# Kernel optimization log

Hardware: AMD Instinct MI355X
Metric: run time of the kernel (lower is better)

Reference implementation:

```python
import jax, jax.numpy as jnp
import numpy as np
from jax import lax


def conv_valid_relu(x, w, b):
    # NHWC valid conv, stride 1, + bias + relu (matches keras Conv2D(..., activation='relu'))
    y = lax.conv_general_dilated(x, w, (1, 1), 'VALID',
                                 dimension_numbers=('NHWC', 'HWIO', 'NHWC'))
    return jax.nn.relu(y + b)


def maxpool2(x):
    # keras MaxPooling2D(): pool 2x2, stride 2, VALID
    return lax.reduce_window(x, -jnp.inf, lax.max, (1, 2, 2, 1), (1, 2, 2, 1), 'VALID')


def affine_bilinear(img, theta):
    # img: [H, W, C]; theta: [6] = (a0..a5).
    # tf.raw_ops.ImageProjectiveTransformV3 semantics (a6=a7=0):
    #   x_in = a0*x_out + a1*y_out + a2;  y_in = a3*x_out + a4*y_out + a5
    # BILINEAR interp; each of the 4 neighbor reads returns fill_value(=0) if out of bounds.
    H, W, C = img.shape
    a0, a1, a2, a3, a4, a5 = theta
    ys, xs = jnp.meshgrid(jnp.arange(H, dtype=img.dtype),
                          jnp.arange(W, dtype=img.dtype), indexing='ij')
    xq = a0 * xs + a1 * ys + a2  # [H, W]
    yq = a3 * xs + a4 * ys + a5
    x0 = jnp.floor(xq)
    y0 = jnp.floor(yq)
    dx = xq - x0
    dy = yq - y0

    def read(yi, xi):
        valid = (yi >= 0) & (yi <= H - 1) & (xi >= 0) & (xi <= W - 1)
        yc = jnp.clip(yi, 0, H - 1).astype(jnp.int32)
        xc = jnp.clip(xi, 0, W - 1).astype(jnp.int32)
        v = img[yc, xc]  # gather -> [H, W, C]
        return jnp.where(valid[..., None], v, jnp.zeros((), img.dtype))

    v00 = read(y0, x0)
    v01 = read(y0, x0 + 1)
    v10 = read(y0 + 1, x0)
    v11 = read(y0 + 1, x0 + 1)
    top = v00 * (1 - dx)[..., None] + v01 * dx[..., None]
    bot = v10 * (1 - dx)[..., None] + v11 * dx[..., None]
    return top * (1 - dy)[..., None] + bot * dy[..., None]


def reference(x, conv1_w, conv1_b, conv2_w, conv2_b, fc_w, fc_b):
    y = conv_valid_relu(x, conv1_w, conv1_b)   # [B,218,218,8]
    y = maxpool2(y)                            # [B,109,109,8]
    y = conv_valid_relu(y, conv2_w, conv2_b)   # [B,105,105,10]
    y = maxpool2(y)                            # [B,52,52,10]
    feat = y.reshape(y.shape[0], -1)           # row-major HWC flatten == keras Flatten
    theta = feat @ fc_w + fc_b                 # [B,6]
    return jax.vmap(affine_bilinear)(x, theta)


def setup_inputs() -> dict:
    key = jax.random.key(0)
    ks = jax.random.split(key, 6)
    B, H, W, C = 64, 224, 224, 3
    flat_dim = 52 * 52 * 10  # from 224 -> conv7 -> pool -> conv5 -> pool
    x = jax.random.normal(ks[0], (B, H, W, C), dtype=jnp.float32)
    conv1_w = jax.random.normal(ks[1], (7, 7, 3, 8), dtype=jnp.float32) * 0.05
    conv1_b = jnp.zeros((8,), jnp.float32)
    conv2_w = jax.random.normal(ks[2], (5, 5, 8, 10), dtype=jnp.float32) * 0.05
    conv2_b = jnp.zeros((10,), jnp.float32)
    # keras init: kernel zeros, bias = identity affine. Add tiny noise to kernel so the
    # predicted transform actually varies per image (exercises the resampler).
    fc_w = jax.random.normal(ks[3], (flat_dim, 6), dtype=jnp.float32) * 1e-4
    fc_b = jnp.array([1.0, 0.0, 0.0, 0.0, 1.0, 0.0], dtype=jnp.float32)
    return {"x": x, "conv1_w": conv1_w, "conv1_b": conv1_b,
            "conv2_w": conv2_w, "conv2_b": conv2_b, "fc_w": fc_w, "fc_b": fc_b}
```

## Files before the change

### kernel.cpp

```cpp
#include <hip/hip_runtime.h>
#include <math.h>

#define BATCH 64
#define HI 224
#define WI 224
#define P1H 109
#define P1W 109
#define P2H 52
#define P2W 52

typedef _Float16 f16;
typedef _Float16 f16x4 __attribute__((ext_vector_type(4)));
typedef _Float16 f16x8 __attribute__((ext_vector_type(8)));
typedef float    f32x4 __attribute__((ext_vector_type(4)));

#define MFMA16F(a,b,c) __builtin_amdgcn_mfma_f32_16x16x32_f16((a),(b),(c),0,0,0)

#define PROWS 4
#define NROWG 28
#define SROWS 14
#define ROWSH 896
#define STOT  (SROWS*ROWSH)
#define SPAD  12576
#define NBVAR 8
__global__ __launch_bounds__(256) void conv1_kernel(
    const float* __restrict__ x, const float* __restrict__ w1,
    const float* __restrict__ b1,
    f16* __restrict__ p1)
{
    __shared__ f16 smem[SPAD + NBVAR*16*32];
    f16* sh_a = smem;
    f16* sh_b = smem + SPAD;

    const int tid  = threadIdx.x;
    const int lane = tid & 63;
    const int wave = tid >> 6;
    const int bph  = blockIdx.x;
    const int b    = blockIdx.y;
    const int ph0  = PROWS*bph;
    const int ir0  = 2*ph0;

    for (int i = tid; i < NBVAR*16*32; i += 256) sh_b[i] = (f16)0.f;
    __syncthreads();

    for (int i = tid; i < 1176; i += 256) {
        const float v = w1[i];
        const int co = i & 7;
        const int t3 = i >> 3;
        const int ci = t3 % 3;
        const int kk = t3 / 3;
        const int kh = kk / 7;
        const int kw = kk - kh*7;
        const f16 val = (f16)v;
        sh_b[(kh*16     + co  )*32 + kw*4 + ci] = val;
        sh_b[((kh+1)*16 + co+8)*32 + kw*4 + ci] = val;
    }

    for (int u = wave; u < 25; u += 4) {
        const int q = u*512 + lane*8;
        if (q >= SPAD) continue;
        const int row  = q / ROWSH;
        const int rem  = q - row*ROWSH;
        const int col0 = rem >> 2;
        const int ira  = ir0 + row;
        float f0=0.f,f1=0.f,f2=0.f,f3=0.f,f4=0.f,f5=0.f;
        if (q < STOT && ira < HI) {
            const float* src = x + ((size_t)(b*HI + ira)*WI + col0)*3;
            const float2 a = *(const float2*)(src);
            const float2 c = *(const float2*)(src+2);
            const float2 e = *(const float2*)(src+4);
            f0=a.x; f1=a.y; f2=c.x; f3=c.y; f4=e.x; f5=e.y;
        }
        f16x8 hv;
        hv[0]=(f16)f0; hv[1]=(f16)f1; hv[2]=(f16)f2; hv[3]=(f16)0.f;
        hv[4]=(f16)f3; hv[5]=(f16)f4; hv[6]=(f16)f5; hv[7]=(f16)0.f;
        *(f16x8*)(sh_a + q) = hv;
    }
    __syncthreads();

    const int n16 = lane & 15;
    const int g   = lane >> 4;

    f16x8 bv[NBVAR];
#pragma unroll
    for (int v = 0; v < NBVAR; ++v)
        bv[v] = *(const f16x8*)(sh_b + (v*16 + n16)*32 + g*8);
    const float bias = b1[n16 & 7];

    for (int t = wave; t < 14; t += 4) {
        const int abase = (t*16 + n16)*4 + g*8;
        f32x4 acc[4];
#pragma unroll
        for (int q = 0; q < 4; ++q) acc[q] = (f32x4){0.f,0.f,0.f,0.f};

#pragma unroll
        for (int ir = 0; ir < SROWS; ++ir) {
            const int sb = ir*ROWSH + abase;
            const f16x4 h0 = *(const f16x4*)(sh_a + sb);
            const f16x4 h1 = *(const f16x4*)(sh_a + sb + 4);
            const f16x8 ah = __builtin_shufflevector(h0,h1,0,1,2,3,4,5,6,7);
#pragma unroll
            for (int q = 0; q < 4; ++q) {
                const int v = ir - 2*q;
                if (v >= 0 && v < NBVAR)
                    acc[q] = MFMA16F(ah, bv[v], acc[q]);
            }
        }

#pragma unroll
        for (int pr = 0; pr < PROWS; ++pr) {
            const float h0 = fmaxf(acc[pr][0], acc[pr][1]);
            const float h1 = fmaxf(acc[pr][2], acc[pr][3]);
            const float v0 = fmaxf(h0, __shfl_xor(h0, 8));
            const float v1 = fmaxf(h1, __shfl_xor(h1, 8));
            const int ph = ph0 + pr;
            if (n16 < 8 && ph < P1H) {
                const int pc0 = t*8 + 2*g;
                const size_t rbase = ((size_t)(b*P1H + ph))*P1W*8;
                if (pc0 < P1W)
                    p1[rbase + (size_t)pc0*8 + n16] = (f16)fmaxf(v0 + bias, 0.f);
                if (pc0+1 < P1W)
                    p1[rbase + (size_t)(pc0+1)*8 + n16] = (f16)fmaxf(v1 + bias, 0.f);
            }
        }
    }
}

#define C2A 6144
__global__ __launch_bounds__(256) void conv2_kernel(
    const f16* __restrict__ p1,
    const float* __restrict__ w2, const float* __restrict__ b2,
    float* __restrict__ p2)
{
    __shared__ f16 smem[C2A + 16*224];
    f16* sh_a = smem;
    f16* sh_b = smem + C2A;

    const int tid = threadIdx.x;
    const int ph  = blockIdx.x;
    const int b   = blockIdx.y;

    for (int i = tid; i < 16*224; i += 256) sh_b[i] = (f16)0.f;
    for (int i = tid; i < C2A - 5232; i += 256) sh_a[5232 + i] = (f16)0.f;
    __syncthreads();

    for (int i = tid; i < 2000; i += 256) {
        const float v = w2[i];
        const int kh = i / 400;
        int rem = i - kh*400;
        const int kw = rem / 80;
        rem -= kw*80;
        const int ci = rem / 10;
        const int co = rem - ci*10;
        sh_b[co*224 + kh*40 + kw*8 + ci] = (f16)v;
    }

    const size_t gbase = ((size_t)b*P1H + 2*ph) * (P1W*8);
    const ulong2* gsrc = (const ulong2*)(p1 + gbase);
    ulong2* gdst = (ulong2*)sh_a;
    for (int c = tid; c < 654; c += 256) gdst[c] = gsrc[c];
    __syncthreads();

    const int lane = tid & 63;
    const int wave = tid >> 6;
    const int n16  = lane & 15;
    const int g    = lane >> 4;

    f16x8 bh[7];
#pragma unroll
    for (int j = 0; j < 7; ++j)
        bh[j] = *(const f16x8*)(sh_b + n16*224 + j*32 + g*8);
    const float bias = (n16 < 10) ? b2[n16] : 0.f;

    int koff[7];
#pragma unroll
    for (int j = 0; j < 7; ++j) {
        const int chunk = 4*j + g;
        const int kh = chunk / 5;
        const int kw = chunk - kh*5;
        koff[j] = kh*872 + kw*8;
    }

    for (int t = wave; t < 7; t += 4) {
        const int c0 = t*16;
        const int pbase = (c0 + n16)*8;
        float res[2][4];
#pragma unroll
        for (int ro = 0; ro < 2; ++ro) {
            f32x4 accA = {0.f,0.f,0.f,0.f};
            f32x4 accB = {0.f,0.f,0.f,0.f};
            const int rb = ro*872 + pbase;
#pragma unroll
            for (int j = 0; j < 7; ++j) {
                const int si = rb + koff[j];
                const f16x8 ah = *(const f16x8*)(sh_a + si);
                if (j & 1) accB = MFMA16F(ah, bh[j], accB);
                else       accA = MFMA16F(ah, bh[j], accA);
            }
#pragma unroll
            for (int r = 0; r < 4; ++r) res[ro][r] = accA[r] + accB[r];
        }
        if (n16 < 10) {
#pragma unroll
            for (int q = 0; q < 2; ++q) {
                const int pc = (c0 >> 1) + 2*g + q;
                if (pc < P2W) {
                    float m = fmaxf(fmaxf(res[0][2*q], res[0][2*q+1]),
                                    fmaxf(res[1][2*q], res[1][2*q+1]));
                    p2[((size_t)((b*P2H + ph)*P2W) + pc)*10 + n16] = fmaxf(m + bias, 0.f);
                }
            }
        }
    }
}

#define FCSL 16
#define FCCH 1690
__global__ __launch_bounds__(256) void fcA_kernel(
    const float* __restrict__ p2, const float* __restrict__ fw,
    float* __restrict__ partial)
{
    const int s = blockIdx.x;
    const int b = blockIdx.y;
    const int base = s * FCCH;
    const float* f = p2 + (size_t)b*27040;
    float acc[6] = {0.f,0.f,0.f,0.f,0.f,0.f};
    for (int i = threadIdx.x; i < FCCH; i += 256) {
        const float v = f[base + i];
        const float* wp = fw + (size_t)(base + i)*6;
#pragma unroll
        for (int k = 0; k < 6; ++k) acc[k] = fmaf(v, wp[k], acc[k]);
    }
    __shared__ float red[4][6];
#pragma unroll
    for (int k = 0; k < 6; ++k) {
        float v = acc[k];
        for (int off = 32; off > 0; off >>= 1) v += __shfl_down(v, off);
        if ((threadIdx.x & 63) == 0) red[threadIdx.x >> 6][k] = v;
    }
    __syncthreads();
    if (threadIdx.x < 6) {
        const int k = threadIdx.x;
        partial[(b*FCSL + s)*6 + k] = red[0][k] + red[1][k] + red[2][k] + red[3][k];
    }
}

__global__ __launch_bounds__(384) void fcB_kernel(
    const float* __restrict__ partial, const float* __restrict__ fb,
    float* __restrict__ theta)
{
    const int t = threadIdx.x;
    const int b = t / 6, k = t - b*6;
    float s = fb[k];
#pragma unroll
    for (int j = 0; j < FCSL; ++j) s += partial[(b*FCSL + j)*6 + k];
    theta[b*6 + k] = s;
}

__global__ __launch_bounds__(256) void resample_kernel(
    const float* __restrict__ x, const float* __restrict__ theta,
    float* __restrict__ out)
{
    const int idx = blockIdx.x * 256 + threadIdx.x;
    const int total = BATCH * HI * WI;
    if (idx >= total) return;
    const int b   = idx / (HI*WI);
    const int pix = idx - b * (HI*WI);
    const int yo  = pix / WI;
    const int xo  = pix - yo * WI;

    const float* t = theta + b*6;
    const float a0 = t[0], a1 = t[1], a2 = t[2], a3 = t[3], a4 = t[4], a5 = t[5];

    const float fx = (float)xo, fy = (float)yo;
    const float xq = a0*fx + a1*fy + a2;
    const float yq = a3*fx + a4*fy + a5;
    const float x0f = floorf(xq), y0f = floorf(yq);
    const float dx = xq - x0f, dy = yq - y0f;
    const int x0 = (int)x0f, y0 = (int)y0f;

    const float* img = x + (size_t)b * (HI*WI*3);

    const int x1 = x0 + 1, y1 = y0 + 1;
    const bool vx0 = (x0 >= 0) && (x0 <= WI-1);
    const bool vx1 = (x1 >= 0) && (x1 <= WI-1);
    const bool vy0 = (y0 >= 0) && (y0 <= HI-1);
    const bool vy1 = (y1 >= 0) && (y1 <= HI-1);
    const int xc0 = min(max(x0, 0), WI-1);
    const int xc1 = min(max(x1, 0), WI-1);
    const int yc0 = min(max(y0, 0), HI-1);
    const int yc1 = min(max(y1, 0), HI-1);
    const float* p00 = img + (size_t)(yc0*WI + xc0)*3;
    const float* p01 = img + (size_t)(yc0*WI + xc1)*3;
    const float* p10 = img + (size_t)(yc1*WI + xc0)*3;
    const float* p11 = img + (size_t)(yc1*WI + xc1)*3;
    const float m00 = (vy0 && vx0) ? 1.f : 0.f;
    const float m01 = (vy0 && vx1) ? 1.f : 0.f;
    const float m10 = (vy1 && vx0) ? 1.f : 0.f;
    const float m11 = (vy1 && vx1) ? 1.f : 0.f;

    float* op = out + (size_t)idx * 3;
#pragma unroll
    for (int c = 0; c < 3; ++c) {
        const float v00 = m00 * p00[c];
        const float v01 = m01 * p01[c];
        const float v10 = m10 * p10[c];
        const float v11 = m11 * p11[c];
        const float top = v00 * (1.f - dx) + v01 * dx;
        const float bot = v10 * (1.f - dx) + v11 * dx;
        op[c] = top * (1.f - dy) + bot * dy;
    }
}

extern "C" void kernel_launch(void* const* d_in, const int* in_sizes, int n_in,
                              void* d_out, int out_size, void* d_ws, size_t ws_size,
                              hipStream_t stream) {
    const float* x   = (const float*)d_in[0];
    const float* w1  = (const float*)d_in[1];
    const float* b1  = (const float*)d_in[2];
    const float* w2  = (const float*)d_in[3];
    const float* b2  = (const float*)d_in[4];
    const float* fw  = (const float*)d_in[5];
    const float* fb  = (const float*)d_in[6];
    float* out = (float*)d_out;

    char* ws = (char*)d_ws;
    f16*  p1      = (f16*)ws;
    float* p2     = (float*)(ws + 12166144);
    float* partial= (float*)(ws + 19088384);
    float* th     = (float*)(ws + 19113000 - 19113000 % 256 + 256);

    conv1_kernel<<<dim3(NROWG, BATCH), 256, 0, stream>>>(x, w1, b1, p1);
    conv2_kernel<<<dim3(P2H, BATCH), 256, 0, stream>>>(p1, w2, b2, p2);
    fcA_kernel<<<dim3(FCSL, BATCH), 256, 0, stream>>>(p2, fw, partial);
    fcB_kernel<<<dim3(1), 384, 0, stream>>>(partial, fb, th);

    const int total_pix = BATCH * HI * WI;
    resample_kernel<<<dim3((total_pix + 255)/256), 256, 0, stream>>>(x, th, out);
}
```

Measured before the change: 73.41 us.

## Stage conv outputs in shared memory and vectorize resample stores

conv1 and conv2 now write their pooled outputs into shared memory, then copy each row to global memory with 16-byte coalesced stores, replacing scattered 2-byte and 4-byte stores. The resample kernel now has each thread compute four consecutive pixels and write twelve floats as three float4 stores, with one image-aligned grid per batch. This trades an extra barrier and some shared-memory staging for better global-store efficiency. conv1 reuses the weight region of shared memory for output staging, so it needs an added sync after the weights are read into registers.

```diff
diff --git a/kernel.cpp b/kernel.cpp
--- a/kernel.cpp
+++ b/kernel.cpp
@@ -8,6 +8,7 @@
 #define P1W 109
 #define P2H 52
 #define P2W 52
+#define NPIX (HI*WI)
 
 typedef _Float16 f16;
 typedef _Float16 f16x4 __attribute__((ext_vector_type(4)));
@@ -29,8 +30,9 @@
     f16* __restrict__ p1)
 {
     __shared__ f16 smem[SPAD + NBVAR*16*32];
-    f16* sh_a = smem;
-    f16* sh_b = smem + SPAD;
+    f16* sh_a   = smem;
+    f16* sh_b   = smem + SPAD;
+    f16* sh_out = smem + SPAD;
 
     const int tid  = threadIdx.x;
     const int lane = tid & 63;
@@ -86,6 +88,7 @@
     for (int v = 0; v < NBVAR; ++v)
         bv[v] = *(const f16x8*)(sh_b + (v*16 + n16)*32 + g*8);
     const float bias = b1[n16 & 7];
+    __syncthreads();
 
     for (int t = wave; t < 14; t += 4) {
         const int abase = (t*16 + n16)*4 + g*8;
@@ -113,16 +116,24 @@
             const float h1 = fmaxf(acc[pr][2], acc[pr][3]);
             const float v0 = fmaxf(h0, __shfl_xor(h0, 8));
             const float v1 = fmaxf(h1, __shfl_xor(h1, 8));
-            const int ph = ph0 + pr;
-            if (n16 < 8 && ph < P1H) {
+            if (n16 < 8) {
                 const int pc0 = t*8 + 2*g;
-                const size_t rbase = ((size_t)(b*P1H + ph))*P1W*8;
                 if (pc0 < P1W)
-                    p1[rbase + (size_t)pc0*8 + n16] = (f16)fmaxf(v0 + bias, 0.f);
+                    sh_out[(pr*P1W + pc0)*8 + n16] = (f16)fmaxf(v0 + bias, 0.f);
                 if (pc0+1 < P1W)
-                    p1[rbase + (size_t)(pc0+1)*8 + n16] = (f16)fmaxf(v1 + bias, 0.f);
+                    sh_out[(pr*P1W + pc0+1)*8 + n16] = (f16)fmaxf(v1 + bias, 0.f);
             }
         }
+    }
+    __syncthreads();
+
+    for (int c = tid; c < PROWS*P1W; c += 256) {
+        const int pr = c / P1W;
+        const int pc = c - pr*P1W;
+        const int ph = ph0 + pr;
+        if (ph < P1H)
+            *(ulong2*)(p1 + ((size_t)(b*P1H + ph)*P1W + pc)*8) =
+                *(const ulong2*)(sh_out + c*8);
     }
 }
 
@@ -133,8 +144,10 @@
     float* __restrict__ p2)
 {
     __shared__ f16 smem[C2A + 16*224];
+    __shared__ float4 sh_o4[130];
     f16* sh_a = smem;
     f16* sh_b = smem + C2A;
+    float* sh_o = (float*)sh_o4;
 
     const int tid = threadIdx.x;
     const int ph  = blockIdx.x;
@@ -207,11 +220,15 @@
                 if (pc < P2W) {
                     float m = fmaxf(fmaxf(res[0][2*q], res[0][2*q+1]),
                                     fmaxf(res[1][2*q], res[1][2*q+1]));
-                    p2[((size_t)((b*P2H + ph)*P2W) + pc)*10 + n16] = fmaxf(m + bias, 0.f);
+                    sh_o[pc*10 + n16] = fmaxf(m + bias, 0.f);
                 }
             }
         }
     }
+    __syncthreads();
+
+    float4* dst = (float4*)(p2 + (size_t)(b*P2H + ph)*520);
+    for (int i = tid; i < 130; i += 256) dst[i] = sh_o4[i];
 }
 
 #define FCSL 16
@@ -261,55 +278,63 @@
     const float* __restrict__ x, const float* __restrict__ theta,
     float* __restrict__ out)
 {
-    const int idx = blockIdx.x * 256 + threadIdx.x;
-    const int total = BATCH * HI * WI;
-    if (idx >= total) return;
-    const int b   = idx / (HI*WI);
-    const int pix = idx - b * (HI*WI);
-    const int yo  = pix / WI;
-    const int xo  = pix - yo * WI;
+    const int u   = blockIdx.x;
+    const int b   = u / 49;
+    const int blk = u - b*49;
+    const int pix0 = blk*1024 + threadIdx.x*4;
 
     const float* t = theta + b*6;
     const float a0 = t[0], a1 = t[1], a2 = t[2], a3 = t[3], a4 = t[4], a5 = t[5];
-
-    const float fx = (float)xo, fy = (float)yo;
-    const float xq = a0*fx + a1*fy + a2;
-    const float yq = a3*fx + a4*fy + a5;
-    const float x0f = floorf(xq), y0f = floorf(yq);
-    const float dx = xq - x0f, dy = yq - y0f;
-    const int x0 = (int)x0f, y0 = (int)y0f;
-
-    const float* img = x + (size_t)b * (HI*WI*3);
-
-    const int x1 = x0 + 1, y1 = y0 + 1;
-    const bool vx0 = (x0 >= 0) && (x0 <= WI-1);
-    const bool vx1 = (x1 >= 0) && (x1 <= WI-1);
-    const bool vy0 = (y0 >= 0) && (y0 <= HI-1);
-    const bool vy1 = (y1 >= 0) && (y1 <= HI-1);
-    const int xc0 = min(max(x0, 0), WI-1);
-    const int xc1 = min(max(x1, 0), WI-1);
-    const int yc0 = min(max(y0, 0), HI-1);
-    const int yc1 = min(max(y1, 0), HI-1);
-    const float* p00 = img + (size_t)(yc0*WI + xc0)*3;
-    const float* p01 = img + (size_t)(yc0*WI + xc1)*3;
-    const float* p10 = img + (size_t)(yc1*WI + xc0)*3;
-    const float* p11 = img + (size_t)(yc1*WI + xc1)*3;
-    const float m00 = (vy0 && vx0) ? 1.f : 0.f;
-    const float m01 = (vy0 && vx1) ? 1.f : 0.f;
-    const float m10 = (vy1 && vx0) ? 1.f : 0.f;
-    const float m11 = (vy1 && vx1) ? 1.f : 0.f;
-
-    float* op = out + (size_t)idx * 3;
-#pragma unroll
-    for (int c = 0; c < 3; ++c) {
-        const float v00 = m00 * p00[c];
-        const float v01 = m01 * p01[c];
-        const float v10 = m10 * p10[c];
-        const float v11 = m11 * p11[c];
-        const float top = v00 * (1.f - dx) + v01 * dx;
-        const float bot = v10 * (1.f - dx) + v11 * dx;
-        op[c] = top * (1.f - dy) + bot * dy;
-    }
+    const float* img = x + (size_t)b * (NPIX*3);
+
+    float o[12];
+#pragma unroll
+    for (int p = 0; p < 4; ++p) {
+        const int pix = pix0 + p;
+        const int yo  = pix / WI;
+        const int xo  = pix - yo * WI;
+
+        const float fx = (float)xo, fy = (float)yo;
+        const float xq = a0*fx + a1*fy + a2;
+        const float yq = a3*fx + a4*fy + a5;
+        const float x0f = floorf(xq), y0f = floorf(yq);
+        const float dx = xq - x0f, dy = yq - y0f;
+        const int x0 = (int)x0f, y0 = (int)y0f;
+
+        const int x1 = x0 + 1, y1 = y0 + 1;
+        const bool vx0 = (x0 >= 0) && (x0 <= WI-1);
+        const bool vx1 = (x1 >= 0) && (x1 <= WI-1);
+        const bool vy0 = (y0 >= 0) && (y0 <= HI-1);
+        const bool vy1 = (y1 >= 0) && (y1 <= HI-1);
+        const int xc0 = min(max(x0, 0), WI-1);
+        const int xc1 = min(max(x1, 0), WI-1);
+        const int yc0 = min(max(y0, 0), HI-1);
+        const int yc1 = min(max(y1, 0), HI-1);
+        const float* p00 = img + (size_t)(yc0*WI + xc0)*3;
+        const float* p01 = img + (size_t)(yc0*WI + xc1)*3;
+        const float* p10 = img + (size_t)(yc1*WI + xc0)*3;
+        const float* p11 = img + (size_t)(yc1*WI + xc1)*3;
+        const float m00 = (vy0 && vx0) ? 1.f : 0.f;
+        const float m01 = (vy0 && vx1) ? 1.f : 0.f;
+        const float m10 = (vy1 && vx0) ? 1.f : 0.f;
+        const float m11 = (vy1 && vx1) ? 1.f : 0.f;
+
+#pragma unroll
+        for (int c = 0; c < 3; ++c) {
+            const float v00 = m00 * p00[c];
+            const float v01 = m01 * p01[c];
+            const float v10 = m10 * p10[c];
+            const float v11 = m11 * p11[c];
+            const float top = v00 * (1.f - dx) + v01 * dx;
+            const float bot = v10 * (1.f - dx) + v11 * dx;
+            o[p*3 + c] = top * (1.f - dy) + bot * dy;
+        }
+    }
+
+    float* op = out + ((size_t)b*NPIX + pix0) * 3;
+    *(float4*)(op + 0) = (float4){o[0], o[1], o[2],  o[3]};
+    *(float4*)(op + 4) = (float4){o[4], o[5], o[6],  o[7]};
+    *(float4*)(op + 8) = (float4){o[8], o[9], o[10], o[11]};
 }
 
 extern "C" void kernel_launch(void* const* d_in, const int* in_sizes, int n_in,
@@ -328,13 +353,12 @@
     f16*  p1      = (f16*)ws;
     float* p2     = (float*)(ws + 12166144);
     float* partial= (float*)(ws + 19088384);
-    float* th     = (float*)(ws + 19113000 - 19113000 % 256 + 256);
+    float* th     = (float*)(ws + 19113216);
 
     conv1_kernel<<<dim3(NROWG, BATCH), 256, 0, stream>>>(x, w1, b1, p1);
     conv2_kernel<<<dim3(P2H, BATCH), 256, 0, stream>>>(p1, w2, b2, p2);
     fcA_kernel<<<dim3(FCSL, BATCH), 256, 0, stream>>>(p2, fw, partial);
     fcB_kernel<<<dim3(1), 384, 0, stream>>>(partial, fb, th);
 
-    const int total_pix = BATCH * HI * WI;
-    resample_kernel<<<dim3((total_pix + 255)/256), 256, 0, stream>>>(x, th, out);
-}
+    resample_kernel<<<dim3(BATCH*49), 256, 0, stream>>>(x, th, out);
+}
```

New measurement: 87.52 us. 1.19x slower.
